# Kernel optimization log

Measured on AMD Instinct MI355X. Metric: run time of the kernel, lower is better.

Reference implementation:

```python
import jax, jax.numpy as jnp
import numpy as np

DEPTH = 4
EPS = 1e-5


def _bn(x, g, b):
    # training-mode BatchNorm over (B,H,W) per channel
    m = x.mean(axis=(0, 2, 3), keepdims=True)
    v = x.var(axis=(0, 2, 3), keepdims=True)
    return (x - m) * jax.lax.rsqrt(v + EPS) * g[None, :, None, None] + b[None, :, None, None]


def _conv_bn(x, w, g, b):
    # 1x1 conv (no bias) + BatchNorm
    y = jnp.einsum('bchw,oc->bohw', x, w)
    return _bn(y, g, b)


def _block_max_broadcast(x, gsz):
    # max over each (H/gsz, W/gsz) block of a gsz x gsz grid, broadcast back
    B, C, H, W = x.shape
    xr = x.reshape(B, C, gsz, H // gsz, gsz, W // gsz)
    m = xr.max(axis=(3, 5), keepdims=True)
    return jnp.broadcast_to(m, xr.shape).reshape(B, C, H, W)


def setup_inputs() -> dict:
    key = jax.random.key(0)
    ks = jax.random.split(key, 3)
    B, C, H, W = 4, 128, 256, 256
    x = jax.random.normal(ks[0], (B, C, H, W), dtype=jnp.float32)
    conv_w = jax.random.normal(ks[1], (DEPTH, C, C), dtype=jnp.float32) * 0.05
    conv_g = jnp.ones((DEPTH, C), dtype=jnp.float32)
    conv_b = jnp.zeros((DEPTH, C), dtype=jnp.float32)
    final_w = jax.random.normal(ks[2], (C, (DEPTH + 1) * C), dtype=jnp.float32) * 0.05
    final_g = jnp.ones((C,), dtype=jnp.float32)
    final_b = jnp.zeros((C,), dtype=jnp.float32)
    return {"x": x, "conv_w": conv_w, "conv_g": conv_g, "conv_b": conv_b,
            "final_w": final_w, "final_g": final_g, "final_b": final_b}


def reference(x, conv_w, conv_g, conv_b, final_w, final_g, final_b):
    # p[0]: identity; p[1+d]: block-max over 2^d x 2^d grid broadcast back, then 1x1 conv+BN
    p = [x]
    for d in range(DEPTH):
        pooled = _block_max_broadcast(x, 2 ** d)  # d=0 -> global max broadcast
        p.append(_conv_bn(pooled, conv_w[d], conv_g[d], conv_b[d]))
    out = jnp.concatenate(p, axis=1)  # [B, 5C, H, W]
    return _conv_bn(out, final_w, final_g, final_b)
```

## Files before the change

### kernel.cpp

```cpp
#include <hip/hip_runtime.h>
#include <hip/hip_bf16.h>
#include <math.h>
#include <float.h>

#define B_ 4
#define C_ 128
#define P_ 65536

#define M3_OFF      0
#define M2_OFF      32768
#define M1_OFF      40960
#define M0_OFF      43008
#define YBASE_      43520
#define SCALED_OFF  87040
#define SHIFTD_OFF  87552
#define CONTRIB_OFF 88064
#define S3_OFF      120832
#define SX_OFF      153600
#define G_OFF       154112
#define SCALEF_OFF  219648
#define SHIFTF_OFF  219776
#define MAXP_OFF    219904
#define SUMP_OFF    744192

using short8 = __attribute__((ext_vector_type(8))) short;
using f32x4 = __attribute__((ext_vector_type(4))) float;
using f32x16 = __attribute__((ext_vector_type(16))) float;

__device__ __forceinline__ int level_rel(int d) {
    return YBASE_ - 512 * (((1 << (2 * (d + 1))) - 1) / 3);
}

__device__ __forceinline__ unsigned int bfpair(float a, float b) {
    unsigned int ua = __float_as_uint(a), ub = __float_as_uint(b);
    ua = (ua + 0x7fffu + ((ua >> 16) & 1u)) >> 16;
    ub = (ub + 0x7fffu + ((ub >> 16) & 1u)) & 0xffff0000u;
    return ua | ub;
}

#define GLDS16(src, dst)                                                    \
    __builtin_amdgcn_global_load_lds(                                       \
        (const __attribute__((address_space(1))) unsigned int*)(src),       \
        (__attribute__((address_space(3))) unsigned int*)(dst), 16, 0, 0)

__device__ __forceinline__ short8 ld_frag(const float* tile, int row, int ks, int l) {
    int ch = ks * 4 + ((l >> 5) << 1);
    int sw = row & 7;
    const float* p0 = tile + row * 128 + ((ch ^ sw) << 2);
    const float* p1 = tile + row * 128 + (((ch + 1) ^ sw) << 2);
    float4 v0 = *(const float4*)p0;
    float4 v1 = *(const float4*)p1;
    union { uint4 u; short8 s; } cu;
    cu.u = make_uint4(bfpair(v0.x, v0.y), bfpair(v0.z, v0.w),
                      bfpair(v1.x, v1.y), bfpair(v1.z, v1.w));
    return cu.s;
}

__global__ __launch_bounds__(256) void k_gram_pool(const float* __restrict__ x,
                                                   float* __restrict__ ws,
                                                   float* __restrict__ gpart) {
    __shared__ float tile[16384];
    int wg = blockIdx.x;
    int b = wg >> 7, rc = wg & 127;
    const float* xb = x + (size_t)b * C_ * P_ + (size_t)rc * 512;
    int t = threadIdx.x, l = t & 63, wv = t >> 6;
    int rhalf = l >> 5;
    int lchunk = l & 31;
    int tc = t >> 2, tjb = t & 3;

    int tr = (wv >> 1) * 64;
    int tcc = (wv & 1) * 64;

    f32x16 acc[2][2];
#pragma unroll
    for (int i = 0; i < 2; ++i)
#pragma unroll
        for (int j = 0; j < 2; ++j)
#pragma unroll
            for (int r = 0; r < 16; ++r) acc[i][j][r] = 0.f;
    float mx[2][2], sm[2][2];
#pragma unroll
    for (int i = 0; i < 2; ++i)
#pragma unroll
        for (int j = 0; j < 2; ++j) { mx[i][j] = -FLT_MAX; sm[i][j] = 0.f; }

#pragma unroll
    for (int s = 0; s < 4; ++s) {
#pragma unroll
        for (int i = 0; i < 16; ++i) {
            int c = wv * 32 + i * 2;
            int row = c + rhalf;
            int chunk = lchunk ^ (row & 7);
            GLDS16(xb + (size_t)row * P_ + s * 128 + chunk * 4, &tile[c * 128]);
        }
        __syncthreads();

#pragma unroll
        for (int ci2 = 0; ci2 < 2; ++ci2) {
            int c = tc + ci2 * 64;
            float m = -FLT_MAX, sum = 0.f;
#pragma unroll
            for (int k = 0; k < 8; ++k) {
                int phys = (tjb * 8 + k) ^ (c & 7);
                float4 v = *(const float4*)(tile + c * 128 + phys * 4);
                m = fmaxf(m, fmaxf(fmaxf(v.x, v.y), fmaxf(v.z, v.w)));
                sum += (v.x + v.y) + (v.z + v.w);
            }
            if ((s & 1) == 0) {
                mx[0][ci2] = fmaxf(mx[0][ci2], m);
                sm[0][ci2] += sum;
            } else {
                mx[1][ci2] = fmaxf(mx[1][ci2], m);
                sm[1][ci2] += sum;
            }
        }

#pragma unroll
        for (int ks = 0; ks < 8; ++ks) {
            short8 af0 = ld_frag(tile, tr + (l & 31), ks, l);
            short8 af1 = ld_frag(tile, tr + 32 + (l & 31), ks, l);
            short8 bf0 = ld_frag(tile, tcc + (l & 31), ks, l);
            short8 bf1 = ld_frag(tile, tcc + 32 + (l & 31), ks, l);
            acc[0][0] = __builtin_amdgcn_mfma_f32_32x32x16_bf16(af0, bf0, acc[0][0], 0, 0, 0);
            acc[0][1] = __builtin_amdgcn_mfma_f32_32x32x16_bf16(af0, bf1, acc[0][1], 0, 0, 0);
            acc[1][0] = __builtin_amdgcn_mfma_f32_32x32x16_bf16(af1, bf0, acc[1][0], 0, 0, 0);
            acc[1][1] = __builtin_amdgcn_mfma_f32_32x32x16_bf16(af1, bf1, acc[1][1], 0, 0, 0);
        }
        __syncthreads();
    }

    size_t gb = (size_t)wg * 16384;
#pragma unroll
    for (int i = 0; i < 2; ++i)
#pragma unroll
        for (int j = 0; j < 2; ++j)
#pragma unroll
            for (int r = 0; r < 16; ++r) {
                int row = tr + i * 32 + (r & 3) + 8 * (r >> 2) + 4 * (l >> 5);
                int col = tcc + j * 32 + (l & 31);
                gpart[gb + (size_t)row * 128 + col] = acc[i][j][r];
            }
    int i3 = rc >> 4, rr = rc & 15;
#pragma unroll
    for (int sp = 0; sp < 2; ++sp)
#pragma unroll
        for (int ci2 = 0; ci2 < 2; ++ci2) {
            int c = tc + ci2 * 64;
            int j3 = sp * 4 + tjb;
            size_t idx = ((size_t)(b * 128 + c) * 64 + i3 * 8 + j3) * 16 + rr;
            ws[MAXP_OFF + idx] = mx[sp][ci2];
            ws[SUMP_OFF + idx] = sm[sp][ci2];
        }
}

__global__ __launch_bounds__(256) void k_reduceG(const float* __restrict__ gpart,
                                                 float* __restrict__ ws) {
    int tid = blockIdx.x * 256 + threadIdx.x;
    int b = tid >> 14, inner = tid & 16383;
    const float* p = gpart + (size_t)b * 128 * 16384 + inner;
    float s = 0.f;
    for (int r = 0; r < 128; ++r) s += p[(size_t)r * 16384];
    ws[G_OFF + tid] = s;
}

__global__ __launch_bounds__(256) void k_reduceMS(float* __restrict__ ws) {
    int bc = blockIdx.x;
    int t = threadIdx.x;
    int blk = t >> 2, q = t & 3;
    __shared__ float bm[64], bs[64];
    __shared__ float lv[24];
    __shared__ float sxr[8];
    {
        size_t base = (size_t)bc * 1024 + blk * 16 + q * 4;
        float4 mv = *(const float4*)(ws + MAXP_OFF + base);
        float4 sv = *(const float4*)(ws + SUMP_OFF + base);
        float m = fmaxf(fmaxf(mv.x, mv.y), fmaxf(mv.z, mv.w));
        float s = (sv.x + sv.y) + (sv.z + sv.w);
        m = fmaxf(m, __shfl_xor(m, 1)); s += __shfl_xor(s, 1);
        m = fmaxf(m, __shfl_xor(m, 2)); s += __shfl_xor(s, 2);
        if (q == 0) {
            bm[blk] = m;
            bs[blk] = s;
            ws[M3_OFF + (size_t)bc * 64 + blk] = m;
            ws[S3_OFF + (size_t)bc * 64 + blk] = s;
        }
    }
    __syncthreads();
    if (t < 8) {
        float sx = 0.f;
        for (int r = 0; r < 8; ++r) sx += bs[t * 8 + r];
        sxr[t] = sx;
    }
    if (t < 16) {
        int i2 = t >> 2, j2 = t & 3;
        float m = -FLT_MAX;
        for (int a = 0; a < 2; ++a)
            for (int b2 = 0; b2 < 2; ++b2)
                m = fmaxf(m, bm[(2 * i2 + a) * 8 + 2 * j2 + b2]);
        lv[t] = m;
        ws[M2_OFF + (size_t)bc * 16 + t] = m;
    }
    __syncthreads();
    if (t == 0) {
        float sx = 0.f;
        for (int r = 0; r < 8; ++r) sx += sxr[r];
        ws[SX_OFF + bc] = sx;
    }
    if (t < 4) {
        int i1 = t >> 1, j1 = t & 1;
        float m = -FLT_MAX;
        for (int a = 0; a < 2; ++a)
            for (int b2 = 0; b2 < 2; ++b2)
                m = fmaxf(m, lv[(2 * i1 + a) * 4 + 2 * j1 + b2]);
        lv[16 + t] = m;
        ws[M1_OFF + (size_t)bc * 4 + t] = m;
    }
    __syncthreads();
    if (t == 0)
        ws[M0_OFF + bc] = fmaxf(fmaxf(lv[16], lv[17]), fmaxf(lv[18], lv[19]));
}

__global__ __launch_bounds__(256) void k_conv_pool(const float* __restrict__ conv_w,
                                                   float* __restrict__ ws) {
    int bid = blockIdx.x;
    int d = bid >> 4, b = (bid >> 2) & 3, cchunk = bid & 3;
    int NB = 1 << (2 * d);
    int rel = level_rel(d);
    const float* Mb = ws + rel + (size_t)b * 128 * NB;
    float* Yb = ws + YBASE_ + rel + (size_t)b * 128 * NB;
    __shared__ float mlds[8192];
    int t = threadIdx.x;
    int tot = 128 * NB;
    for (int i = t; i < tot; i += 256) mlds[i] = Mb[i];
    __syncthreads();
    if (NB >= 4) {
        int nbq = NB >> 2;
        int nq = 32 * nbq;
        for (int qi = t; qi < nq; qi += 256) {
            int co = cchunk * 32 + (qi >> (2 * d - 2));
            int bq = qi & (nbq - 1);
            const float* wrow = conv_w + ((size_t)d * 128 + co) * 128;
            float a0 = 0.f, a1 = 0.f, a2 = 0.f, a3 = 0.f;
            for (int ci = 0; ci < 128; ++ci) {
                float4 mv = *(const float4*)(&mlds[ci * NB + bq * 4]);
                float wvv = wrow[ci];
                a0 = fmaf(wvv, mv.x, a0);
                a1 = fmaf(wvv, mv.y, a1);
                a2 = fmaf(wvv, mv.z, a2);
                a3 = fmaf(wvv, mv.w, a3);
            }
            float4 r;
            r.x = a0; r.y = a1; r.z = a2; r.w = a3;
            *(float4*)(&Yb[co * NB + bq * 4]) = r;
        }
    } else {
        for (int oi = t; oi < 32; oi += 256) {
            int co = cchunk * 32 + oi;
            const float* wrow = conv_w + (size_t)co * 128;
            float acc = 0.f;
            for (int ci = 0; ci < 128; ++ci) acc = fmaf(mlds[ci], wrow[ci], acc);
            Yb[co] = acc;
        }
    }
}

__global__ __launch_bounds__(256) void k_bnstats_d(const float* __restrict__ conv_g,
                                                   const float* __restrict__ conv_b,
                                                   float* __restrict__ ws) {
    int tid = blockIdx.x * 256 + threadIdx.x;
    if (tid >= 512) return;
    int d = tid >> 7, c = tid & 127;
    int NB = 1 << (2 * d);
    const float* Y = ws + YBASE_ + level_rel(d);
    int n = 4 * NB;
    float s = 0.f;
    for (int b = 0; b < 4; ++b)
        for (int k = 0; k < NB; ++k) s += Y[((size_t)b * 128 + c) * NB + k];
    float mean = s / (float)n;
    float v = 0.f;
    for (int b = 0; b < 4; ++b)
        for (int k = 0; k < NB; ++k) {
            float dd = Y[((size_t)b * 128 + c) * NB + k] - mean;
            v = fmaf(dd, dd, v);
        }
    float var = v / (float)n;
    float sc = conv_g[d * 128 + c] * rsqrtf(var + 1e-5f);
    ws[SCALED_OFF + tid] = sc;
    ws[SHIFTD_OFF + tid] = conv_b[d * 128 + c] - mean * sc;
}

__global__ __launch_bounds__(128) void k_contrib(const float* __restrict__ final_w,
                                                 float* __restrict__ ws) {
    int b = blockIdx.x >> 6, blk3 = blockIdx.x & 63;
    int i3 = blk3 >> 3, j3 = blk3 & 7;
    __shared__ float pn[512];
    int t = threadIdx.x;
    for (int k = t; k < 512; k += 128) {
        int d = k >> 7, c = k & 127;
        int sh = 3 - d;
        int blkd = (i3 >> sh) * (1 << d) + (j3 >> sh);
        int NB = 1 << (2 * d);
        float yv = ws[YBASE_ + level_rel(d) + ((size_t)b * 128 + c) * NB + blkd];
        pn[k] = yv * ws[SCALED_OFF + k] + ws[SHIFTD_OFF + k];
    }
    __syncthreads();
    const float* fw = final_w + (size_t)t * 640 + 128;
    float acc = 0.f;
#pragma unroll 8
    for (int k = 0; k < 512; k += 4) {
        float4 f = *(const float4*)(fw + k);
        acc = fmaf(pn[k], f.x, acc);
        acc = fmaf(pn[k + 1], f.y, acc);
        acc = fmaf(pn[k + 2], f.z, acc);
        acc = fmaf(pn[k + 3], f.w, acc);
    }
    ws[CONTRIB_OFF + ((size_t)b * 128 + t) * 64 + blk3] = acc;
}

__global__ __launch_bounds__(128) void k_stats(const float* __restrict__ final_w,
                                               const float* __restrict__ final_g,
                                               const float* __restrict__ final_b,
                                               float* __restrict__ ws) {
    int o = blockIdx.x, t = threadIdx.x;
    __shared__ __align__(16) float wlds[128];
    __shared__ __align__(16) float cvl[64];
    __shared__ float rbuf[4];
    wlds[t] = final_w[(size_t)o * 640 + t];
    __syncthreads();
    float SSQ = 0.f, SUM = 0.f;
    for (int b = 0; b < 4; ++b) {
        if (t < 64) cvl[t] = ws[CONTRIB_OFF + (size_t)(b * 128 + o) * 64 + t];
        __syncthreads();
        const float* Gb = ws + G_OFF + (size_t)b * 16384 + (size_t)t * 128;
        float a1 = 0.f;
#pragma unroll 8
        for (int k = 0; k < 128; k += 4) {
            float4 g = *(const float4*)(Gb + k);
            float4 w = *(const float4*)(&wlds[k]);
            a1 = fmaf(g.x, w.x, fmaf(g.y, w.y, fmaf(g.z, w.z, fmaf(g.w, w.w, a1))));
        }
        const float* S3p = ws + S3_OFF + (size_t)(b * 128 + t) * 64;
        float a2 = 0.f;
#pragma unroll 8
        for (int k = 0; k < 64; k += 4) {
            float4 sv = *(const float4*)(S3p + k);
            float4 cv = *(const float4*)(&cvl[k]);
            a2 = fmaf(sv.x, cv.x, fmaf(sv.y, cv.y, fmaf(sv.z, cv.z, fmaf(sv.w, cv.w, a2))));
        }
        float r1 = (a1 + 2.f * a2) * wlds[t];
        float r2 = wlds[t] * ws[SX_OFF + b * 128 + t];
        if (t < 64) {
            r1 += 1024.f * cvl[t] * cvl[t];
            r2 += 1024.f * cvl[t];
        }
#pragma unroll
        for (int k = 1; k < 64; k <<= 1) {
            r1 += __shfl_xor(r1, k);
            r2 += __shfl_xor(r2, k);
        }
        if ((t & 63) == 0) {
            rbuf[(t >> 6) * 2] = r1;
            rbuf[(t >> 6) * 2 + 1] = r2;
        }
        __syncthreads();
        SSQ += rbuf[0] + rbuf[2];
        SUM += rbuf[1] + rbuf[3];
        __syncthreads();
    }
    if (t == 0) {
        float mean = SUM / 262144.f;
        float var = SSQ / 262144.f - mean * mean;
        float sc = final_g[o] * rsqrtf(var + 1e-5f);
        ws[SCALEF_OFF + o] = sc;
        ws[SHIFTF_OFF + o] = final_b[o] - mean * sc;
    }
}

__global__ __launch_bounds__(256) void k_out(const float* __restrict__ x,
                                             const float* __restrict__ final_w,
                                             const float* __restrict__ ws,
                                             float* __restrict__ out) {
    __shared__ uint4 wtileq[2048];
    __shared__ float scl[128], shf[128], cvs[512];
    unsigned char* wtile = (unsigned char*)wtileq;
    int wgid = blockIdx.x;
    int b = wgid >> 9, pt = wgid & 511;
    int p0 = pt * 128;
    int t = threadIdx.x, l = t & 63, wv = t >> 6;
#pragma unroll
    for (int it = 0; it < 32; ++it) {
        int pid = it * 256 + t;
        int o = pid >> 6, cp = (pid & 63) * 2;
        float2 f = *(const float2*)(final_w + (size_t)o * 640 + cp);
        unsigned int u = bfpair(f.x, f.y);
        int wa = (o * 256 + cp * 2) ^ ((o & 7) << 4);
        *(unsigned int*)(wtile + wa) = u;
    }
    if (t < 128) {
        scl[t] = ws[SCALEF_OFF + t];
        shf[t] = ws[SHIFTF_OFF + t];
    }
    int i3 = pt >> 6, jb = (pt & 1) * 4;
    for (int q = t; q < 512; q += 256) {
        int o = q >> 2, jj = q & 3;
        cvs[q] = ws[CONTRIB_OFF + (size_t)(b * 128 + o) * 64 + i3 * 8 + jb + jj];
    }
    __syncthreads();

    const float* xb = x + (size_t)b * C_ * P_;
    int pw = p0 + wv * 32;
    f32x4 acc[8][2];
#pragma unroll
    for (int i = 0; i < 8; ++i) {
        acc[i][0] = (f32x4){0.f, 0.f, 0.f, 0.f};
        acc[i][1] = (f32x4){0.f, 0.f, 0.f, 0.f};
    }
#pragma unroll
    for (int ks = 0; ks < 4; ++ks) {
        short8 bf[2];
#pragma unroll
        for (int nt = 0; nt < 2; ++nt) {
            const float* xp = xb + (size_t)(ks * 32 + (l >> 4) * 8) * P_ + (pw + nt * 16 + (l & 15));
            float f0 = xp[0 * P_], f1 = xp[1 * P_], f2 = xp[2 * P_], f3 = xp[3 * P_];
            float f4 = xp[4 * P_], f5 = xp[5 * P_], f6 = xp[6 * P_], f7 = xp[7 * P_];
            union { uint4 u; short8 s; } cvtu;
            cvtu.u = make_uint4(bfpair(f0, f1), bfpair(f2, f3), bfpair(f4, f5), bfpair(f6, f7));
            bf[nt] = cvtu.s;
        }
#pragma unroll
        for (int mt = 0; mt < 8; ++mt) {
            int ra = ((mt * 16 + (l & 15)) * 256 + ks * 64 + (l >> 4) * 16) ^ ((l & 7) << 4);
            short8 af = *(const short8*)(wtile + ra);
            acc[mt][0] = __builtin_amdgcn_mfma_f32_16x16x32_bf16(af, bf[0], acc[mt][0], 0, 0, 0);
            acc[mt][1] = __builtin_amdgcn_mfma_f32_16x16x32_bf16(af, bf[1], acc[mt][1], 0, 0, 0);
        }
    }
#pragma unroll
    for (int mt = 0; mt < 8; ++mt)
#pragma unroll
        for (int nt = 0; nt < 2; ++nt) {
            int p = pw + nt * 16 + (l & 15);
            int jj = ((p & 255) >> 5) & 3;
#pragma unroll
            for (int r = 0; r < 4; ++r) {
                int o = mt * 16 + (l >> 4) * 4 + r;
                float z = acc[mt][nt][r] + cvs[o * 4 + jj];
                out[(size_t)(b * 128 + o) * P_ + p] = fmaf(z, scl[o], shf[o]);
            }
        }
}

extern "C" void kernel_launch(void* const* d_in, const int* in_sizes, int n_in,
                              void* d_out, int out_size, void* d_ws, size_t ws_size,
                              hipStream_t stream) {
    const float* x = (const float*)d_in[0];
    const float* conv_w = (const float*)d_in[1];
    const float* conv_g = (const float*)d_in[2];
    const float* conv_b = (const float*)d_in[3];
    const float* final_w = (const float*)d_in[4];
    const float* final_g = (const float*)d_in[5];
    const float* final_b = (const float*)d_in[6];
    float* out = (float*)d_out;
    float* ws = (float*)d_ws;

    k_gram_pool<<<512, 256, 0, stream>>>(x, ws, out);
    k_reduceG<<<256, 256, 0, stream>>>(out, ws);
    k_reduceMS<<<512, 256, 0, stream>>>(ws);
    k_conv_pool<<<64, 256, 0, stream>>>(conv_w, ws);
    k_bnstats_d<<<2, 256, 0, stream>>>(conv_g, conv_b, ws);
    k_contrib<<<B_ * 64, 128, 0, stream>>>(final_w, ws);
    k_stats<<<128, 128, 0, stream>>>(final_w, final_g, final_b, ws);
    k_out<<<2048, 256, 0, stream>>>(x, final_w, ws, out);
}
```

Measured before the change: 211.0 us.

## Double-buffer gram tile loads and fuse pooling stats into fragment reads

The gram/pool kernel now stages the input in two 64-column LDS buffers and prefetches the next slice while the current one feeds the MFMAs, replacing the single 128-column buffer that was loaded and waited on each step. The separate max/sum pooling pass over LDS is removed. Instead, the even waves compute block max and sum from the same float4 values they already read for the A fragments, then combine the two lane halves with cross-lane shuffles. This cuts redundant LDS reads and hides global load latency, at the cost of more accumulator registers (32 max/sum values per lane) and a tighter coupling between pooling layout and MFMA fragment layout.

After: 196.1 us. 1.08x faster.

```diff
diff --git a/kernel.cpp b/kernel.cpp
--- a/kernel.cpp
+++ b/kernel.cpp
@@ -43,33 +43,17 @@
         (const __attribute__((address_space(1))) unsigned int*)(src),       \
         (__attribute__((address_space(3))) unsigned int*)(dst), 16, 0, 0)
 
-__device__ __forceinline__ short8 ld_frag(const float* tile, int row, int ks, int l) {
-    int ch = ks * 4 + ((l >> 5) << 1);
-    int sw = row & 7;
-    const float* p0 = tile + row * 128 + ((ch ^ sw) << 2);
-    const float* p1 = tile + row * 128 + (((ch + 1) ^ sw) << 2);
-    float4 v0 = *(const float4*)p0;
-    float4 v1 = *(const float4*)p1;
-    union { uint4 u; short8 s; } cu;
-    cu.u = make_uint4(bfpair(v0.x, v0.y), bfpair(v0.z, v0.w),
-                      bfpair(v1.x, v1.y), bfpair(v1.z, v1.w));
-    return cu.s;
-}
-
 __global__ __launch_bounds__(256) void k_gram_pool(const float* __restrict__ x,
                                                    float* __restrict__ ws,
                                                    float* __restrict__ gpart) {
-    __shared__ float tile[16384];
+    __shared__ float tile[2][8192];
     int wg = blockIdx.x;
     int b = wg >> 7, rc = wg & 127;
     const float* xb = x + (size_t)b * C_ * P_ + (size_t)rc * 512;
     int t = threadIdx.x, l = t & 63, wv = t >> 6;
-    int rhalf = l >> 5;
-    int lchunk = l & 31;
-    int tc = t >> 2, tjb = t & 3;
-
     int tr = (wv >> 1) * 64;
     int tcc = (wv & 1) * 64;
+    bool doacc = ((wv & 1) == 0);
 
     f32x16 acc[2][2];
 #pragma unroll
@@ -78,53 +62,61 @@
         for (int j = 0; j < 2; ++j)
 #pragma unroll
             for (int r = 0; r < 16; ++r) acc[i][j][r] = 0.f;
-    float mx[2][2], sm[2][2];
+    float mxA[2][8], smA[2][8];
 #pragma unroll
     for (int i = 0; i < 2; ++i)
 #pragma unroll
-        for (int j = 0; j < 2; ++j) { mx[i][j] = -FLT_MAX; sm[i][j] = 0.f; }
-
-#pragma unroll
-    for (int s = 0; s < 4; ++s) {
-#pragma unroll
-        for (int i = 0; i < 16; ++i) {
-            int c = wv * 32 + i * 2;
-            int row = c + rhalf;
-            int chunk = lchunk ^ (row & 7);
-            GLDS16(xb + (size_t)row * P_ + s * 128 + chunk * 4, &tile[c * 128]);
-        }
-        __syncthreads();
-
-#pragma unroll
-        for (int ci2 = 0; ci2 < 2; ++ci2) {
-            int c = tc + ci2 * 64;
-            float m = -FLT_MAX, sum = 0.f;
-#pragma unroll
-            for (int k = 0; k < 8; ++k) {
-                int phys = (tjb * 8 + k) ^ (c & 7);
-                float4 v = *(const float4*)(tile + c * 128 + phys * 4);
-                m = fmaxf(m, fmaxf(fmaxf(v.x, v.y), fmaxf(v.z, v.w)));
-                sum += (v.x + v.y) + (v.z + v.w);
-            }
-            if ((s & 1) == 0) {
-                mx[0][ci2] = fmaxf(mx[0][ci2], m);
-                sm[0][ci2] += sum;
-            } else {
-                mx[1][ci2] = fmaxf(mx[1][ci2], m);
-                sm[1][ci2] += sum;
-            }
-        }
-
-#pragma unroll
-        for (int ks = 0; ks < 8; ++ks) {
-            short8 af0 = ld_frag(tile, tr + (l & 31), ks, l);
-            short8 af1 = ld_frag(tile, tr + 32 + (l & 31), ks, l);
-            short8 bf0 = ld_frag(tile, tcc + (l & 31), ks, l);
-            short8 bf1 = ld_frag(tile, tcc + 32 + (l & 31), ks, l);
-            acc[0][0] = __builtin_amdgcn_mfma_f32_32x32x16_bf16(af0, bf0, acc[0][0], 0, 0, 0);
-            acc[0][1] = __builtin_amdgcn_mfma_f32_32x32x16_bf16(af0, bf1, acc[0][1], 0, 0, 0);
-            acc[1][0] = __builtin_amdgcn_mfma_f32_32x32x16_bf16(af1, bf0, acc[1][0], 0, 0, 0);
-            acc[1][1] = __builtin_amdgcn_mfma_f32_32x32x16_bf16(af1, bf1, acc[1][1], 0, 0, 0);
+        for (int j = 0; j < 8; ++j) { mxA[i][j] = -FLT_MAX; smA[i][j] = 0.f; }
+
+#pragma unroll
+    for (int i = 0; i < 8; ++i) {
+        int row = wv * 32 + i * 4 + (l >> 4);
+        int chunk = (l & 15) ^ (row & 15);
+        GLDS16(xb + (size_t)row * P_ + chunk * 4, &tile[0][(wv * 32 + i * 4) * 64]);
+    }
+    __syncthreads();
+
+#pragma unroll
+    for (int s = 0; s < 8; ++s) {
+        if (s < 7) {
+#pragma unroll
+            for (int i = 0; i < 8; ++i) {
+                int row = wv * 32 + i * 4 + (l >> 4);
+                int chunk = (l & 15) ^ (row & 15);
+                GLDS16(xb + (size_t)row * P_ + (s + 1) * 64 + chunk * 4,
+                       &tile[(s + 1) & 1][(wv * 32 + i * 4) * 64]);
+            }
+        }
+        const float* tl = &tile[s & 1][0];
+#pragma unroll
+        for (int ks = 0; ks < 4; ++ks) {
+            int jci = 2 * (s & 3) + (ks >> 1);
+            int ch = ks * 4 + ((l >> 5) << 1);
+            short8 fr[4];
+#pragma unroll
+            for (int fi = 0; fi < 4; ++fi) {
+                int row = (fi < 2 ? tr : tcc) + (fi & 1) * 32 + (l & 31);
+                int sw = row & 15;
+                const float* p0 = tl + row * 64 + ((ch ^ sw) << 2);
+                const float* p1 = tl + row * 64 + (((ch + 1) ^ sw) << 2);
+                float4 v0 = *(const float4*)p0;
+                float4 v1 = *(const float4*)p1;
+                if (fi < 2 && doacc) {
+                    mxA[fi][jci] = fmaxf(mxA[fi][jci],
+                        fmaxf(fmaxf(fmaxf(v0.x, v0.y), fmaxf(v0.z, v0.w)),
+                              fmaxf(fmaxf(v1.x, v1.y), fmaxf(v1.z, v1.w))));
+                    smA[fi][jci] += ((v0.x + v0.y) + (v0.z + v0.w)) +
+                                    ((v1.x + v1.y) + (v1.z + v1.w));
+                }
+                union { uint4 u; short8 s8; } cu;
+                cu.u = make_uint4(bfpair(v0.x, v0.y), bfpair(v0.z, v0.w),
+                                  bfpair(v1.x, v1.y), bfpair(v1.z, v1.w));
+                fr[fi] = cu.s8;
+            }
+            acc[0][0] = __builtin_amdgcn_mfma_f32_32x32x16_bf16(fr[0], fr[2], acc[0][0], 0, 0, 0);
+            acc[0][1] = __builtin_amdgcn_mfma_f32_32x32x16_bf16(fr[0], fr[3], acc[0][1], 0, 0, 0);
+            acc[1][0] = __builtin_amdgcn_mfma_f32_32x32x16_bf16(fr[1], fr[2], acc[1][0], 0, 0, 0);
+            acc[1][1] = __builtin_amdgcn_mfma_f32_32x32x16_bf16(fr[1], fr[3], acc[1][1], 0, 0, 0);
         }
         __syncthreads();
     }
@@ -140,17 +132,23 @@
                 int col = tcc + j * 32 + (l & 31);
                 gpart[gb + (size_t)row * 128 + col] = acc[i][j][r];
             }
-    int i3 = rc >> 4, rr = rc & 15;
-#pragma unroll
-    for (int sp = 0; sp < 2; ++sp)
-#pragma unroll
-        for (int ci2 = 0; ci2 < 2; ++ci2) {
-            int c = tc + ci2 * 64;
-            int j3 = sp * 4 + tjb;
-            size_t idx = ((size_t)(b * 128 + c) * 64 + i3 * 8 + j3) * 16 + rr;
-            ws[MAXP_OFF + idx] = mx[sp][ci2];
-            ws[SUMP_OFF + idx] = sm[sp][ci2];
-        }
+    if (doacc) {
+        int i3 = rc >> 4, rr = rc & 15;
+#pragma unroll
+        for (int half = 0; half < 2; ++half)
+#pragma unroll
+            for (int jc = 0; jc < 8; ++jc) {
+                float m = mxA[half][jc], sv = smA[half][jc];
+                m = fmaxf(m, __shfl_xor(m, 32));
+                sv += __shfl_xor(sv, 32);
+                if (l < 32) {
+                    int c = tr + half * 32 + l;
+                    size_t idx = ((size_t)(b * 128 + c) * 64 + i3 * 8 + jc) * 16 + rr;
+                    ws[MAXP_OFF + idx] = m;
+                    ws[SUMP_OFF + idx] = sv;
+                }
+            }
+    }
 }
 
 __global__ __launch_bounds__(256) void k_reduceG(const float* __restrict__ gpart,
```
